# Kernel optimization log

Measured on AMD Instinct MI355X. Metric: run time of the kernel, lower is better.

## Reference

```python
import jax, jax.numpy as jnp
from jax import lax
import numpy as np

KH, KW = 7, 7


def setup_inputs() -> dict:
    key = jax.random.key(0)
    kx, _ = jax.random.split(key)
    x = jax.random.uniform(kx, (32, 3, 1024, 1024), dtype=jnp.float32)
    # Box kernel of ones; normalization (normalized=True) happens in reference.
    kernel = jnp.ones((KH, KW), dtype=jnp.float32)
    return {"x": x, "kernel": kernel}


def reference(x, kernel):
    # BoxBlur: normalized box kernel, reflect padding, depthwise 2D conv.
    kh, kw = kernel.shape
    k = kernel / jnp.sum(kernel)  # L1-normalized box kernel (normalized=True)
    # reflect padding by k//2 on each spatial side (kornia compute_padding for odd k)
    xp = jnp.pad(x, ((0, 0), (0, 0), (kh // 2, kh // 2), (kw // 2, kw // 2)), mode="reflect")
    C = x.shape[1]
    w = jnp.broadcast_to(k[None, None], (C, 1, kh, kw))  # depthwise: one kernel per channel
    out = lax.conv_general_dilated(
        xp, w,
        window_strides=(1, 1),
        padding="VALID",
        dimension_numbers=("NCHW", "OIHW", "NCHW"),
        feature_group_count=C,
    )
    return out
```

## Files before the change

### kernel.cpp

```cpp
#include <hip/hip_runtime.h>

#define BH 128
#define NB 8

typedef float f32x4 __attribute__((ext_vector_type(4)));

__device__ __forceinline__ int reflect_idx(int i, int n) {
    if (i < 0) i = -i;
    if (i >= n) i = 2 * n - 2 - i;
    return i;
}

__device__ __forceinline__ float4 ld4(const float* p) {
    return *reinterpret_cast<const float4*>(p);
}

struct Row3 { float4 A, B, C; };

__device__ __forceinline__ Row3 load_row3(const float* __restrict__ row, int x0,
                                          bool xlo, bool xhi) {
    Row3 r;
    r.B = ld4(row + x0);
    const float* pa = row + (xlo ? x0 : x0 - 4);
    const float* pc = row + (xhi ? x0 : x0 + 4);
    r.A = ld4(pa);
    r.C = ld4(pc);
    return r;
}

__device__ __forceinline__ float4 hsum_fix(Row3 t, bool xlo, bool xhi) {
    if (xlo) t.A = make_float4(t.C.x, t.B.w, t.B.z, t.B.y);
    if (xhi) t.C = make_float4(t.B.z, t.B.y, t.B.x, t.A.w);
    float h0 = t.A.y + t.A.z + t.A.w + t.B.x + t.B.y + t.B.z + t.B.w;
    float h1 = h0 - t.A.y + t.C.x;
    float h2 = h1 - t.A.z + t.C.y;
    float h3 = h2 - t.A.w + t.C.z;
    return make_float4(h0, h1, h2, h3);
}

__global__ __launch_bounds__(256, 3) void boxblur_kernel(const float* __restrict__ in,
                                                         float* __restrict__ out,
                                                         int H, int W, int cpx) {
    const int bid = blockIdx.x;
    const int sbid = (bid & 7) * cpx + (bid >> 3);
    const int plane = sbid >> 3;
    const int y0 = (sbid & 7) * BH;

    const float* __restrict__ src = in + (size_t)plane * H * W;
    float* __restrict__ dst = out + (size_t)plane * H * W;

    const int x0 = threadIdx.x * 4;
    const bool xlo = (x0 == 0), xhi = (x0 + 4 == W);

    float4 hr[8];
    float4 vs = make_float4(0.f, 0.f, 0.f, 0.f);
#pragma unroll
    for (int j = 0; j < 7; ++j) {
        const float* rp = src + (size_t)reflect_idx(y0 - 4 + j, H) * W;
        float4 h = hsum_fix(load_row3(rp, x0, xlo, xhi), xlo, xhi);
        hr[1 + j] = h;
        vs.x += h.x; vs.y += h.y; vs.z += h.z; vs.w += h.w;
    }

    Row3 s0 = load_row3(src + (size_t)reflect_idx(y0 + 3, H) * W, x0, xlo, xhi);
    Row3 s1 = load_row3(src + (size_t)reflect_idx(y0 + 4, H) * W, x0, xlo, xhi);
    Row3 s2 = load_row3(src + (size_t)reflect_idx(y0 + 5, H) * W, x0, xlo, xhi);
    Row3 s3 = load_row3(src + (size_t)reflect_idx(y0 + 6, H) * W, x0, xlo, xhi);
    Row3 s4 = load_row3(src + (size_t)reflect_idx(y0 + 7, H) * W, x0, xlo, xhi);
    Row3 s5 = load_row3(src + (size_t)reflect_idx(y0 + 8, H) * W, x0, xlo, xhi);
    Row3 s6 = load_row3(src + (size_t)reflect_idx(y0 + 9, H) * W, x0, xlo, xhi);
    Row3 s7 = load_row3(src + (size_t)reflect_idx(y0 + 10, H) * W, x0, xlo, xhi);

    const float inv = 1.0f / 49.0f;
    float* orow = dst + (size_t)y0 * W + x0;
    int yload = y0 + 11;

#define PHASE(p, pn)                                                              \
    {                                                                             \
        float4 hn = hsum_fix(s##p, xlo, xhi);                                     \
        vs.x += hn.x - hr[pn].x; vs.y += hn.y - hr[pn].y;                         \
        vs.z += hn.z - hr[pn].z; vs.w += hn.w - hr[pn].w;                         \
        hr[p] = hn;                                                               \
        f32x4 o = { vs.x * inv, vs.y * inv, vs.z * inv, vs.w * inv };             \
        __builtin_nontemporal_store(o, reinterpret_cast<f32x4*>(orow));           \
        orow += W;                                                                \
        s##p = load_row3(src + (size_t)reflect_idx(yload, H) * W, x0, xlo, xhi);  \
        ++yload;                                                                  \
    }

    for (int it = 0; it < BH / 8; ++it) {
        PHASE(0, 1) PHASE(1, 2) PHASE(2, 3) PHASE(3, 4)
        PHASE(4, 5) PHASE(5, 6) PHASE(6, 7) PHASE(7, 0)
    }
#undef PHASE
}

extern "C" void kernel_launch(void* const* d_in, const int* in_sizes, int n_in,
                              void* d_out, int out_size, void* d_ws, size_t ws_size,
                              hipStream_t stream) {
    const float* x = (const float*)d_in[0];
    float* out = (float*)d_out;
    const int H = 1024, W = 1024;
    const int NC = 32 * 3;
    const int nwg = NC * NB;
    dim3 grid(nwg);
    dim3 block(256);
    boxblur_kernel<<<grid, block, 0, stream>>>(x, out, H, W, nwg / 8);
}
```

Measured before the change: 176.2 us.

## Process eight columns per thread with 64-row bands and shallower prefetch

Each thread now computes eight output columns instead of four. This cuts the redundant halo loads per output (four float4 loads per 8 outputs instead of three per 4), and the horizontal running sum now spans eight outputs. Blocks shrink to 128 threads and bands to 64 rows, doubling the block count. The row prefetch ring drops from eight rows to four to hold register pressure down. The tradeoffs are more halo rows re-read per band, fewer loads in flight, and a larger per-thread register footprint.

Result: slower. 246.7 us (+40.0%).

```diff
diff --git a/kernel.cpp b/kernel.cpp
--- a/kernel.cpp
+++ b/kernel.cpp
@@ -1,7 +1,7 @@
 #include <hip/hip_runtime.h>
 
-#define BH 128
-#define NB 8
+#define BH 64
+#define NBANDS 16
 
 typedef float f32x4 __attribute__((ext_vector_type(4)));
 
@@ -15,82 +15,97 @@
     return *reinterpret_cast<const float4*>(p);
 }
 
-struct Row3 { float4 A, B, C; };
+struct Row4 { float4 A, B1, B2, C; };
+struct H2  { float4 lo, hi; };
 
-__device__ __forceinline__ Row3 load_row3(const float* __restrict__ row, int x0,
+__device__ __forceinline__ Row4 load_row4(const float* __restrict__ row, int x0,
                                           bool xlo, bool xhi) {
-    Row3 r;
-    r.B = ld4(row + x0);
+    Row4 r;
+    r.B1 = ld4(row + x0);
+    r.B2 = ld4(row + x0 + 4);
     const float* pa = row + (xlo ? x0 : x0 - 4);
-    const float* pc = row + (xhi ? x0 : x0 + 4);
+    const float* pc = row + (xhi ? x0 : x0 + 8);
     r.A = ld4(pa);
     r.C = ld4(pc);
     return r;
 }
 
-__device__ __forceinline__ float4 hsum_fix(Row3 t, bool xlo, bool xhi) {
-    if (xlo) t.A = make_float4(t.C.x, t.B.w, t.B.z, t.B.y);
-    if (xhi) t.C = make_float4(t.B.z, t.B.y, t.B.x, t.A.w);
-    float h0 = t.A.y + t.A.z + t.A.w + t.B.x + t.B.y + t.B.z + t.B.w;
-    float h1 = h0 - t.A.y + t.C.x;
-    float h2 = h1 - t.A.z + t.C.y;
-    float h3 = h2 - t.A.w + t.C.z;
-    return make_float4(h0, h1, h2, h3);
+__device__ __forceinline__ H2 hsum_fix(Row4 t, bool xlo, bool xhi) {
+    if (xlo) t.A = make_float4(t.B2.x, t.B1.w, t.B1.z, t.B1.y);
+    if (xhi) t.C = make_float4(t.B2.z, t.B2.y, t.B2.x, t.B1.w);
+    float r1 = t.A.y,  r2 = t.A.z,  r3 = t.A.w;
+    float r4 = t.B1.x, r5 = t.B1.y, r6 = t.B1.z, r7 = t.B1.w;
+    float r8 = t.B2.x, r9 = t.B2.y, r10 = t.B2.z, r11 = t.B2.w;
+    float r12 = t.C.x, r13 = t.C.y, r14 = t.C.z;
+    float h0 = r1 + r2 + r3 + r4 + r5 + r6 + r7;
+    float h1 = h0 - r1 + r8;
+    float h2 = h1 - r2 + r9;
+    float h3 = h2 - r3 + r10;
+    float h4 = h3 - r4 + r11;
+    float h5 = h4 - r5 + r12;
+    float h6 = h5 - r6 + r13;
+    float h7 = h6 - r7 + r14;
+    H2 o;
+    o.lo = make_float4(h0, h1, h2, h3);
+    o.hi = make_float4(h4, h5, h6, h7);
+    return o;
 }
 
-__global__ __launch_bounds__(256, 3) void boxblur_kernel(const float* __restrict__ in,
+__global__ __launch_bounds__(128, 3) void boxblur_kernel(const float* __restrict__ in,
                                                          float* __restrict__ out,
                                                          int H, int W, int cpx) {
     const int bid = blockIdx.x;
     const int sbid = (bid & 7) * cpx + (bid >> 3);
-    const int plane = sbid >> 3;
-    const int y0 = (sbid & 7) * BH;
+    const int plane = sbid >> 4;
+    const int y0 = (sbid & 15) * BH;
 
     const float* __restrict__ src = in + (size_t)plane * H * W;
     float* __restrict__ dst = out + (size_t)plane * H * W;
 
-    const int x0 = threadIdx.x * 4;
-    const bool xlo = (x0 == 0), xhi = (x0 + 4 == W);
+    const int x0 = threadIdx.x * 8;
+    const bool xlo = (x0 == 0), xhi = (x0 + 8 == W);
 
-    float4 hr[8];
-    float4 vs = make_float4(0.f, 0.f, 0.f, 0.f);
+    float4 hrl[8], hrh[8];
+    float4 vl = make_float4(0.f, 0.f, 0.f, 0.f);
+    float4 vh = make_float4(0.f, 0.f, 0.f, 0.f);
 #pragma unroll
     for (int j = 0; j < 7; ++j) {
         const float* rp = src + (size_t)reflect_idx(y0 - 4 + j, H) * W;
-        float4 h = hsum_fix(load_row3(rp, x0, xlo, xhi), xlo, xhi);
-        hr[1 + j] = h;
-        vs.x += h.x; vs.y += h.y; vs.z += h.z; vs.w += h.w;
+        H2 h = hsum_fix(load_row4(rp, x0, xlo, xhi), xlo, xhi);
+        hrl[1 + j] = h.lo; hrh[1 + j] = h.hi;
+        vl.x += h.lo.x; vl.y += h.lo.y; vl.z += h.lo.z; vl.w += h.lo.w;
+        vh.x += h.hi.x; vh.y += h.hi.y; vh.z += h.hi.z; vh.w += h.hi.w;
     }
 
-    Row3 s0 = load_row3(src + (size_t)reflect_idx(y0 + 3, H) * W, x0, xlo, xhi);
-    Row3 s1 = load_row3(src + (size_t)reflect_idx(y0 + 4, H) * W, x0, xlo, xhi);
-    Row3 s2 = load_row3(src + (size_t)reflect_idx(y0 + 5, H) * W, x0, xlo, xhi);
-    Row3 s3 = load_row3(src + (size_t)reflect_idx(y0 + 6, H) * W, x0, xlo, xhi);
-    Row3 s4 = load_row3(src + (size_t)reflect_idx(y0 + 7, H) * W, x0, xlo, xhi);
-    Row3 s5 = load_row3(src + (size_t)reflect_idx(y0 + 8, H) * W, x0, xlo, xhi);
-    Row3 s6 = load_row3(src + (size_t)reflect_idx(y0 + 9, H) * W, x0, xlo, xhi);
-    Row3 s7 = load_row3(src + (size_t)reflect_idx(y0 + 10, H) * W, x0, xlo, xhi);
+    Row4 s0 = load_row4(src + (size_t)reflect_idx(y0 + 3, H) * W, x0, xlo, xhi);
+    Row4 s1 = load_row4(src + (size_t)reflect_idx(y0 + 4, H) * W, x0, xlo, xhi);
+    Row4 s2 = load_row4(src + (size_t)reflect_idx(y0 + 5, H) * W, x0, xlo, xhi);
+    Row4 s3 = load_row4(src + (size_t)reflect_idx(y0 + 6, H) * W, x0, xlo, xhi);
 
     const float inv = 1.0f / 49.0f;
     float* orow = dst + (size_t)y0 * W + x0;
-    int yload = y0 + 11;
+    int yload = y0 + 7;
 
-#define PHASE(p, pn)                                                              \
+#define PHASE(p, praw, pn)                                                        \
     {                                                                             \
-        float4 hn = hsum_fix(s##p, xlo, xhi);                                     \
-        vs.x += hn.x - hr[pn].x; vs.y += hn.y - hr[pn].y;                         \
-        vs.z += hn.z - hr[pn].z; vs.w += hn.w - hr[pn].w;                         \
-        hr[p] = hn;                                                               \
-        f32x4 o = { vs.x * inv, vs.y * inv, vs.z * inv, vs.w * inv };             \
-        __builtin_nontemporal_store(o, reinterpret_cast<f32x4*>(orow));           \
+        H2 hn = hsum_fix(s##praw, xlo, xhi);                                      \
+        vl.x += hn.lo.x - hrl[pn].x; vl.y += hn.lo.y - hrl[pn].y;                 \
+        vl.z += hn.lo.z - hrl[pn].z; vl.w += hn.lo.w - hrl[pn].w;                 \
+        vh.x += hn.hi.x - hrh[pn].x; vh.y += hn.hi.y - hrh[pn].y;                 \
+        vh.z += hn.hi.z - hrh[pn].z; vh.w += hn.hi.w - hrh[pn].w;                 \
+        hrl[p] = hn.lo; hrh[p] = hn.hi;                                           \
+        f32x4 o1 = { vl.x * inv, vl.y * inv, vl.z * inv, vl.w * inv };            \
+        f32x4 o2 = { vh.x * inv, vh.y * inv, vh.z * inv, vh.w * inv };            \
+        __builtin_nontemporal_store(o1, reinterpret_cast<f32x4*>(orow));          \
+        __builtin_nontemporal_store(o2, reinterpret_cast<f32x4*>(orow + 4));      \
         orow += W;                                                                \
-        s##p = load_row3(src + (size_t)reflect_idx(yload, H) * W, x0, xlo, xhi);  \
+        s##praw = load_row4(src + (size_t)reflect_idx(yload, H) * W, x0, xlo, xhi); \
         ++yload;                                                                  \
     }
 
     for (int it = 0; it < BH / 8; ++it) {
-        PHASE(0, 1) PHASE(1, 2) PHASE(2, 3) PHASE(3, 4)
-        PHASE(4, 5) PHASE(5, 6) PHASE(6, 7) PHASE(7, 0)
+        PHASE(0, 0, 1) PHASE(1, 1, 2) PHASE(2, 2, 3) PHASE(3, 3, 4)
+        PHASE(4, 0, 5) PHASE(5, 1, 6) PHASE(6, 2, 7) PHASE(7, 3, 0)
     }
 #undef PHASE
 }
@@ -102,8 +117,8 @@
     float* out = (float*)d_out;
     const int H = 1024, W = 1024;
     const int NC = 32 * 3;
-    const int nwg = NC * NB;
+    const int nwg = NC * NBANDS;
     dim3 grid(nwg);
-    dim3 block(256);
+    dim3 block(128);
     boxblur_kernel<<<grid, block, 0, stream>>>(x, out, H, W, nwg / 8);
 }
```

## Fetch horizontal halo via wavefront shuffles instead of redundant neighbor loads

Applied to the files above, without the earlier changes.

Each thread now loads only its own float4 per row and gets the three left and three right neighbor values from adjacent lanes with shuffle-up and shuffle-down. Only the edge lanes of each wavefront issue extra halo loads, and reflect handling now keys on thread index. The row prefetch depth also drops from 8 to 4 slots, which saves registers. The aim is to cut vector memory instructions per row roughly threefold. The cost is cross-lane shuffle instructions and a shorter prefetch pipeline, which may expose more memory latency.

New measurement: 165.9 us. 5.8% less time.

```diff
diff --git a/kernel.cpp b/kernel.cpp
--- a/kernel.cpp
+++ b/kernel.cpp
@@ -15,26 +15,34 @@
     return *reinterpret_cast<const float4*>(p);
 }
 
-struct Row3 { float4 A, B, C; };
+struct Slot { float4 B, Ae, Ce; };
 
-__device__ __forceinline__ Row3 load_row3(const float* __restrict__ row, int x0,
-                                          bool xlo, bool xhi) {
-    Row3 r;
-    r.B = ld4(row + x0);
-    const float* pa = row + (xlo ? x0 : x0 - 4);
-    const float* pc = row + (xhi ? x0 : x0 + 4);
-    r.A = ld4(pa);
-    r.C = ld4(pc);
-    return r;
+__device__ __forceinline__ Slot load_slot(const float* __restrict__ row, int x0,
+                                          bool welo, bool wehi) {
+    Slot s;
+    s.B = ld4(row + x0);
+    if (welo) s.Ae = ld4(row + x0 - 4);
+    if (wehi) s.Ce = ld4(row + x0 + 4);
+    return s;
 }
 
-__device__ __forceinline__ float4 hsum_fix(Row3 t, bool xlo, bool xhi) {
-    if (xlo) t.A = make_float4(t.C.x, t.B.w, t.B.z, t.B.y);
-    if (xhi) t.C = make_float4(t.B.z, t.B.y, t.B.x, t.A.w);
-    float h0 = t.A.y + t.A.z + t.A.w + t.B.x + t.B.y + t.B.z + t.B.w;
-    float h1 = h0 - t.A.y + t.C.x;
-    float h2 = h1 - t.A.z + t.C.y;
-    float h3 = h2 - t.A.w + t.C.z;
+__device__ __forceinline__ float4 hsum_slot(const Slot& s,
+                                            bool welo, bool wehi, bool xlo, bool xhi) {
+    const float4 B = s.B;
+    float rm3 = __shfl_up(B.y, 1);
+    float rm2 = __shfl_up(B.z, 1);
+    float rm1 = __shfl_up(B.w, 1);
+    float rp1 = __shfl_down(B.x, 1);
+    float rp2 = __shfl_down(B.y, 1);
+    float rp3 = __shfl_down(B.z, 1);
+    if (welo) { rm3 = s.Ae.y; rm2 = s.Ae.z; rm1 = s.Ae.w; }
+    if (xlo)  { rm3 = B.w;    rm2 = B.z;    rm1 = B.y;    }
+    if (wehi) { rp1 = s.Ce.x; rp2 = s.Ce.y; rp3 = s.Ce.z; }
+    if (xhi)  { rp1 = B.z;    rp2 = B.y;    rp3 = B.x;    }
+    float h0 = rm3 + rm2 + rm1 + B.x + B.y + B.z + B.w;
+    float h1 = h0 - rm3 + rp1;
+    float h2 = h1 - rm2 + rp2;
+    float h3 = h2 - rm1 + rp3;
     return make_float4(h0, h1, h2, h3);
 }
 
@@ -49,48 +57,48 @@
     const float* __restrict__ src = in + (size_t)plane * H * W;
     float* __restrict__ dst = out + (size_t)plane * H * W;
 
-    const int x0 = threadIdx.x * 4;
-    const bool xlo = (x0 == 0), xhi = (x0 + 4 == W);
+    const int tid = threadIdx.x;
+    const int x0 = tid * 4;
+    const int lane = tid & 63;
+    const bool xlo = (tid == 0), xhi = (tid == 255);
+    const bool welo = (lane == 0) && !xlo;
+    const bool wehi = (lane == 63) && !xhi;
 
     float4 hr[8];
     float4 vs = make_float4(0.f, 0.f, 0.f, 0.f);
 #pragma unroll
     for (int j = 0; j < 7; ++j) {
         const float* rp = src + (size_t)reflect_idx(y0 - 4 + j, H) * W;
-        float4 h = hsum_fix(load_row3(rp, x0, xlo, xhi), xlo, xhi);
+        float4 h = hsum_slot(load_slot(rp, x0, welo, wehi), welo, wehi, xlo, xhi);
         hr[1 + j] = h;
         vs.x += h.x; vs.y += h.y; vs.z += h.z; vs.w += h.w;
     }
 
-    Row3 s0 = load_row3(src + (size_t)reflect_idx(y0 + 3, H) * W, x0, xlo, xhi);
-    Row3 s1 = load_row3(src + (size_t)reflect_idx(y0 + 4, H) * W, x0, xlo, xhi);
-    Row3 s2 = load_row3(src + (size_t)reflect_idx(y0 + 5, H) * W, x0, xlo, xhi);
-    Row3 s3 = load_row3(src + (size_t)reflect_idx(y0 + 6, H) * W, x0, xlo, xhi);
-    Row3 s4 = load_row3(src + (size_t)reflect_idx(y0 + 7, H) * W, x0, xlo, xhi);
-    Row3 s5 = load_row3(src + (size_t)reflect_idx(y0 + 8, H) * W, x0, xlo, xhi);
-    Row3 s6 = load_row3(src + (size_t)reflect_idx(y0 + 9, H) * W, x0, xlo, xhi);
-    Row3 s7 = load_row3(src + (size_t)reflect_idx(y0 + 10, H) * W, x0, xlo, xhi);
+    Slot s0 = load_slot(src + (size_t)reflect_idx(y0 + 3, H) * W, x0, welo, wehi);
+    Slot s1 = load_slot(src + (size_t)reflect_idx(y0 + 4, H) * W, x0, welo, wehi);
+    Slot s2 = load_slot(src + (size_t)reflect_idx(y0 + 5, H) * W, x0, welo, wehi);
+    Slot s3 = load_slot(src + (size_t)reflect_idx(y0 + 6, H) * W, x0, welo, wehi);
 
     const float inv = 1.0f / 49.0f;
     float* orow = dst + (size_t)y0 * W + x0;
-    int yload = y0 + 11;
+    int yload = y0 + 7;
 
-#define PHASE(p, pn)                                                              \
-    {                                                                             \
-        float4 hn = hsum_fix(s##p, xlo, xhi);                                     \
-        vs.x += hn.x - hr[pn].x; vs.y += hn.y - hr[pn].y;                         \
-        vs.z += hn.z - hr[pn].z; vs.w += hn.w - hr[pn].w;                         \
-        hr[p] = hn;                                                               \
-        f32x4 o = { vs.x * inv, vs.y * inv, vs.z * inv, vs.w * inv };             \
-        __builtin_nontemporal_store(o, reinterpret_cast<f32x4*>(orow));           \
-        orow += W;                                                                \
-        s##p = load_row3(src + (size_t)reflect_idx(yload, H) * W, x0, xlo, xhi);  \
-        ++yload;                                                                  \
+#define PHASE(p, praw, pn)                                                          \
+    {                                                                               \
+        float4 hn = hsum_slot(s##praw, welo, wehi, xlo, xhi);                       \
+        vs.x += hn.x - hr[pn].x; vs.y += hn.y - hr[pn].y;                           \
+        vs.z += hn.z - hr[pn].z; vs.w += hn.w - hr[pn].w;                           \
+        hr[p] = hn;                                                                 \
+        f32x4 o = { vs.x * inv, vs.y * inv, vs.z * inv, vs.w * inv };               \
+        __builtin_nontemporal_store(o, reinterpret_cast<f32x4*>(orow));             \
+        orow += W;                                                                  \
+        s##praw = load_slot(src + (size_t)reflect_idx(yload, H) * W, x0, welo, wehi); \
+        ++yload;                                                                    \
     }
 
     for (int it = 0; it < BH / 8; ++it) {
-        PHASE(0, 1) PHASE(1, 2) PHASE(2, 3) PHASE(3, 4)
-        PHASE(4, 5) PHASE(5, 6) PHASE(6, 7) PHASE(7, 0)
+        PHASE(0, 0, 1) PHASE(1, 1, 2) PHASE(2, 2, 3) PHASE(3, 3, 4)
+        PHASE(4, 0, 5) PHASE(5, 1, 6) PHASE(6, 2, 7) PHASE(7, 3, 0)
     }
 #undef PHASE
 }
```
